# Kernel tuning notes

Measured on AMD Instinct MI355X. Metric: run time of the kernel, lower is better.

## Reference

```python
import jax, jax.numpy as jnp
import numpy as np

H, P, N, G, K, CH, E = 32, 128, 128, 8, 4, 256, 2048  # heads, head_dim, ssm_state, groups, conv_kernel, chunk, embed
I = H * P                      # intermediate_size = 4096
CD = I + 2 * G * N             # conv_dim = 6144
PROJ = I + CD + H              # 10272
EPS = 1e-6


def segsum(x):
    # x: [..., L] -> [..., L, L]; entry (i, j) = sum_{k=j+1..i} x[k] for j<=i, else -inf
    L = x.shape[-1]
    cs = jnp.cumsum(x, axis=-1)
    ss = cs[..., :, None] - cs[..., None, :]
    mask = jnp.tril(jnp.ones((L, L), dtype=bool))
    return jnp.where(mask, ss, -jnp.inf)


def setup_inputs() -> dict:
    key = jax.random.key(0)
    ks = jax.random.split(key, 6)
    b, s = 2, 2048
    return {
        'x': jax.random.normal(ks[0], (b, s, E), jnp.float32),
        'in_proj_w': jax.random.normal(ks[1], (PROJ, E), jnp.float32) / np.sqrt(E),
        'conv_w': jax.random.normal(ks[2], (CD, 1, K), jnp.float32) / np.sqrt(K),
        'conv_b': jax.random.normal(ks[3], (CD,), jnp.float32) * 0.02,
        'dt_bias': jax.random.normal(ks[4], (H,), jnp.float32) * 0.1 + 1.0,
        'A_log': jnp.log(jnp.arange(1, H + 1, dtype=jnp.float32)),
        'D': jnp.ones((H,), jnp.float32),
        'norm_w': jnp.ones((I,), jnp.float32),
        'out_proj_w': jax.random.normal(ks[5], (E, I), jnp.float32) / np.sqrt(I),
    }


def reference(x, in_proj_w, conv_w, conv_b, dt_bias, A_log, D, norm_w, out_proj_w):
    b, s, _ = x.shape
    proj = x @ in_proj_w.T                                   # [b,s,PROJ] (d_mlp == 0)
    gate, hbc, dt = jnp.split(proj, [I, I + CD], axis=-1)

    # causal depthwise conv1d (pad k-1 on left == torch pad both + slice [:s])
    hbc_t = jnp.transpose(hbc, (0, 2, 1))                    # [b,CD,s]
    conv = jax.lax.conv_general_dilated(
        hbc_t, conv_w, window_strides=(1,), padding=[(K - 1, 0)],
        feature_group_count=CD, dimension_numbers=('NCH', 'OIH', 'NCH'))
    hbc = jax.nn.silu(jnp.transpose(conv + conv_b[None, :, None], (0, 2, 1)))
    hs, B, C = jnp.split(hbc, [I, I + G * N], axis=-1)

    A = -jnp.exp(A_log.astype(jnp.float32))                  # [H]
    dt = jax.nn.softplus(dt.astype(jnp.float32) + dt_bias)   # [b,s,H]
    dt = jnp.clip(dt, 0.0, None)                             # time_step_limit (0, inf)
    X = hs.reshape(b, s, H, P).astype(jnp.float32)
    B = jnp.tile(B.reshape(b, s, G, N).astype(jnp.float32), (1, 1, H // G, 1))  # torch .repeat
    C = jnp.tile(C.reshape(b, s, G, N).astype(jnp.float32), (1, 1, H // G, 1))

    D_res = D[:, None] * X                                   # [b,s,H,P]
    X = X * dt[..., None]                                    # discretize x
    A_bt = A * dt                                            # [b,s,H] discretized A

    nc = s // CH  # seq_len chosen divisible by chunk_size (pad_size = 0)
    Xc = X.reshape(b, nc, CH, H, P)
    Bc = B.reshape(b, nc, CH, H, N)
    Cc = C.reshape(b, nc, CH, H, N)
    Ac = jnp.transpose(A_bt.reshape(b, nc, CH, H), (0, 3, 1, 2))  # [b,H,nc,CH]
    A_cum = jnp.cumsum(Ac, axis=-1)

    # 1. intra-chunk (diagonal block) outputs
    Lmat = jnp.exp(segsum(Ac))                               # [b,H,nc,l,l]
    Y_diag = jnp.einsum('bclhn,bcshn,bhcls,bcshd->bclhd', Cc, Bc, Lmat, Xc)

    # 2. per-chunk states (right factor of off-diagonal blocks)
    decay_states = jnp.exp(A_cum[..., -1:] - A_cum)          # [b,H,nc,CH]
    states = jnp.einsum('bclhn,bhcl,bclhd->bchdn', Bc, decay_states, Xc)

    # 3. inter-chunk recurrence (states at chunk boundaries)
    states = jnp.concatenate([jnp.zeros_like(states[:, :1]), states], axis=1)
    A_last = jnp.pad(A_cum[..., -1], ((0, 0), (0, 0), (1, 0)))
    decay_chunk = jnp.exp(segsum(A_last))                    # [b,H,nc+1,nc+1]
    new_states = jnp.einsum('bhij,bjhdn->bihdn', decay_chunk, states)
    states_prev = new_states[:, :-1]                         # [b,nc,H,P,N]

    # 4. state -> output (left factor of off-diagonal blocks)
    state_decay = jnp.exp(A_cum)
    Y_off = jnp.einsum('bclhn,bchdn,bhcl->bclhd', Cc, states_prev, state_decay)

    y = (Y_diag + Y_off).reshape(b, s, H, P) + D_res
    y = y.reshape(b, s, I)

    # gated grouped RMSNorm (group_size = I // G = 512, divides I)
    gs = I // G
    h32 = y * jax.nn.silu(gate.astype(jnp.float32))
    g = h32.reshape(b, s, I // gs, gs)
    var = jnp.mean(g * g, axis=-1, keepdims=True)
    h32 = (g * jax.lax.rsqrt(var + EPS)).reshape(b, s, I)
    return (norm_w * h32) @ out_proj_w.T                     # [b,s,E]
```

## Files before the change

### kernel.cpp

```cpp
#include <hip/hip_runtime.h>
#include <stdint.h>

#define Hh 32
#define Pp 128
#define Nn 128
#define Gg 8
#define Kk 4
#define CHc 256
#define Ee 2048
#define Ii 4096
#define CDd 6144
#define Mm 4096
#define NCn 8
#define GNn 1024
#define NG1 10240

using short8  = __attribute__((ext_vector_type(8))) short;
using floatx4 = __attribute__((ext_vector_type(4))) float;

__device__ __forceinline__ unsigned short f2bf(float f) {
  unsigned u = __float_as_uint(f);
  u += 0x7FFF + ((u >> 16) & 1);
  return (unsigned short)(u >> 16);
}
__device__ __forceinline__ float bf2f(unsigned short s) {
  return __uint_as_float(((unsigned)s) << 16);
}
__device__ __forceinline__ void gld_lds16(void* lds, const void* g) {
  __builtin_amdgcn_global_load_lds(
      (const __attribute__((address_space(1))) void*)g,
      (__attribute__((address_space(3))) void*)lds, 16, 0, 0);
}

__global__ void ws_probe(float* out, float mb) { out[0] = mb; }

__global__ __launch_bounds__(256) void cvt_bf16(const float* __restrict__ src,
                                                unsigned short* __restrict__ dst,
                                                size_t n4) {
  size_t i = (size_t)blockIdx.x * 256 + threadIdx.x;
  if (i < n4) {
    float4 v = ((const float4*)src)[i];
    ushort4 o;
    o.x = f2bf(v.x); o.y = f2bf(v.y); o.z = f2bf(v.z); o.w = f2bf(v.w);
    ((ushort4*)dst)[i] = o;
  }
}

__global__ __launch_bounds__(256) void dt_gemv(const float* __restrict__ x,
                                               const float* __restrict__ W1,
                                               float* __restrict__ dtraw) {
  int row = blockIdx.x;
  __shared__ float xs[Ee];
  for (int i = threadIdx.x; i < Ee / 4; i += 256)
    ((float4*)xs)[i] = ((const float4*)(x + (size_t)row * Ee))[i];
  __syncthreads();
  int h = threadIdx.x >> 3, seg = threadIdx.x & 7;
  const float* wr = W1 + (size_t)(NG1 + h) * Ee;
  float s = 0.f;
  for (int k = seg; k < Ee; k += 8) s = fmaf(xs[k], wr[k], s);
  s += __shfl_xor(s, 1);
  s += __shfl_xor(s, 2);
  s += __shfl_xor(s, 4);
  if (seg == 0) dtraw[(size_t)row * Hh + h] = s;
}

#define BM 128
#define BN 128
#define BK 64
__global__ __launch_bounds__(256) void gemm_bt(const unsigned short* __restrict__ A,
                                               const unsigned short* __restrict__ B,
                                               int K, int mode,
                                               float* __restrict__ out_f,
                                               unsigned short* __restrict__ out_gate,
                                               unsigned short* __restrict__ out_hbc,
                                               int Nout) {
  __shared__ unsigned short As[BM * BK];
  __shared__ unsigned short Bs[BN * BK];
  const int tid = threadIdx.x;
  const int wid = tid >> 6, lane = tid & 63;
  const int q = lane >> 4, l16 = lane & 15;
  const int m0 = blockIdx.y * BM;
  const int n0 = blockIdx.x * BN;
  floatx4 acc[8][2] = {};

  const int cb = tid & 192;
  for (int k0 = 0; k0 < K; k0 += BK) {
    __syncthreads();
#pragma unroll
    for (int it = 0; it < 4; ++it) {
      int chunkbase = it * 256 + cb;
      int chunk = chunkbase + lane;
      int m = chunk >> 3, kk = (chunk & 7) << 3;
      gld_lds16(&As[chunkbase * 8], &A[(size_t)(m0 + m) * K + k0 + kk]);
      gld_lds16(&Bs[chunkbase * 8], &B[(size_t)(n0 + m) * K + k0 + kk]);
    }
    __syncthreads();
#pragma unroll
    for (int kk = 0; kk < BK; kk += 32) {
      const int ko = kk + q * 8;
      short8 af[8];
#pragma unroll
      for (int mt = 0; mt < 8; ++mt)
        af[mt] = *(const short8*)&As[(mt * 16 + l16) * BK + ko];
      short8 bf0 = *(const short8*)&Bs[(wid * 32 + l16) * BK + ko];
      short8 bf1 = *(const short8*)&Bs[(wid * 32 + 16 + l16) * BK + ko];
#pragma unroll
      for (int mt = 0; mt < 8; ++mt) {
        acc[mt][0] = __builtin_amdgcn_mfma_f32_16x16x32_bf16(af[mt], bf0, acc[mt][0], 0, 0, 0);
        acc[mt][1] = __builtin_amdgcn_mfma_f32_16x16x32_bf16(af[mt], bf1, acc[mt][1], 0, 0, 0);
      }
    }
  }
#pragma unroll
  for (int mt = 0; mt < 8; ++mt)
#pragma unroll
    for (int nt = 0; nt < 2; ++nt)
#pragma unroll
      for (int r = 0; r < 4; ++r) {
        int row = m0 + mt * 16 + q * 4 + r;
        int col = n0 + wid * 32 + nt * 16 + l16;
        float v = acc[mt][nt][r];
        if (mode == 0) {
          out_f[(size_t)row * Nout + col] = v;
        } else {
          if (col < Ii) out_gate[(size_t)row * Ii + col] = f2bf(v);
          else out_hbc[(size_t)row * CDd + (col - Ii)] = f2bf(v);
        }
      }
}

__global__ __launch_bounds__(256) void conv_silu(const unsigned short* __restrict__ hbc,
                                                 const float* __restrict__ cw,
                                                 const float* __restrict__ cb,
                                                 unsigned short* __restrict__ Xr,
                                                 unsigned short* __restrict__ Bb,
                                                 unsigned short* __restrict__ Cb) {
  int idx = blockIdx.x * 256 + threadIdx.x;
  int c4 = (idx % (CDd / 4)) * 4;
  int row = idx / (CDd / 4);
  int s = row & 2047;
  const unsigned short* base = hbc + (size_t)row * CDd + c4;
  ushort4 zero = {0, 0, 0, 0};
  ushort4 r0 = (s >= 3) ? *(const ushort4*)(base - (size_t)3 * CDd) : zero;
  ushort4 r1 = (s >= 2) ? *(const ushort4*)(base - (size_t)2 * CDd) : zero;
  ushort4 r2 = (s >= 1) ? *(const ushort4*)(base - (size_t)1 * CDd) : zero;
  ushort4 r3 = *(const ushort4*)base;
  float i0[4] = {bf2f(r0.x), bf2f(r0.y), bf2f(r0.z), bf2f(r0.w)};
  float i1[4] = {bf2f(r1.x), bf2f(r1.y), bf2f(r1.z), bf2f(r1.w)};
  float i2[4] = {bf2f(r2.x), bf2f(r2.y), bf2f(r2.z), bf2f(r2.w)};
  float i3[4] = {bf2f(r3.x), bf2f(r3.y), bf2f(r3.z), bf2f(r3.w)};
  ushort4 o;
  unsigned short* op = (unsigned short*)&o;
#pragma unroll
  for (int ch = 0; ch < 4; ++ch) {
    int c = c4 + ch;
    float4 w = *(const float4*)&cw[c * 4];
    float v = cb[c];
    v = fmaf(i0[ch], w.x, v);
    v = fmaf(i1[ch], w.y, v);
    v = fmaf(i2[ch], w.z, v);
    v = fmaf(i3[ch], w.w, v);
    v = v / (1.f + expf(-v));
    op[ch] = f2bf(v);
  }
  if (c4 < Ii) *(ushort4*)&Xr[(size_t)row * Ii + c4] = o;
  else if (c4 < Ii + GNn) *(ushort4*)&Bb[(size_t)row * GNn + (c4 - Ii)] = o;
  else *(ushort4*)&Cb[(size_t)row * GNn + (c4 - Ii - GNn)] = o;
}

__global__ __launch_bounds__(256) void dt_cumsum(const float* __restrict__ dtraw,
                                                 const float* __restrict__ dt_bias,
                                                 const float* __restrict__ A_log,
                                                 float* __restrict__ dtbuf,
                                                 float* __restrict__ Acum) {
  int bc = blockIdx.x;
  int h = blockIdx.y;
  int l = threadIdx.x;
  int row = bc * CHc + l;
  float xv = dtraw[(size_t)row * Hh + h] + dt_bias[h];
  float dt = (xv > 20.f) ? xv : log1pf(expf(xv));
  dtbuf[(size_t)row * Hh + h] = dt;
  float a = -expf(A_log[h]) * dt;
  __shared__ float buf[CHc];
  buf[l] = a;
  __syncthreads();
  for (int off = 1; off < CHc; off <<= 1) {
    float v = (l >= off) ? buf[l - off] : 0.f;
    __syncthreads();
    buf[l] += v;
    __syncthreads();
  }
  Acum[((size_t)bc * Hh + h) * CHc + l] = buf[l];
}

__global__ __launch_bounds__(256, 2) void states_kernel(const unsigned short* __restrict__ Xraw,
                                                        const unsigned short* __restrict__ Bbuf,
                                                        const float* __restrict__ dtbuf,
                                                        const float* __restrict__ Acum,
                                                        unsigned short* __restrict__ states) {
  int bch = blockIdx.x;
  int h = bch & 31, bc = bch >> 5;
  int g = h & 7;
  int rowbase = bc * CHc;
  const float* Ac = Acum + (size_t)bch * CHc;
  __shared__ unsigned short XTt[128 * 136];
  __shared__ unsigned short BTt[128 * 136];
  __shared__ float wl[128];
  int t = threadIdx.x;
  int wid = t >> 6, lane = t & 63, q = lane >> 4, l16 = lane & 15;
  float Alast = Ac[CHc - 1];
  floatx4 acc[8][2] = {};
  for (int lt = 0; lt < 2; ++lt) {
    int l0 = lt * 128;
    if (t < 128)
      wl[t] = dtbuf[(size_t)(rowbase + l0 + t) * Hh + h] * __expf(Alast - Ac[l0 + t]);
    __syncthreads();
    for (int i = t; i < 2048; i += 256) {
      int r = i >> 4, c8 = (i & 15) * 8;
      int row = rowbase + l0 + r;
      const unsigned short* xp = &Xraw[(size_t)row * Ii + h * Pp + c8];
      const unsigned short* bp = &Bbuf[(size_t)row * GNn + g * Nn + c8];
      ushort4 xa = *(const ushort4*)xp;
      ushort4 xb = *(const ushort4*)(xp + 4);
      ushort4 ba = *(const ushort4*)bp;
      ushort4 bb = *(const ushort4*)(bp + 4);
      float w = wl[r];
      XTt[(c8 + 0) * 136 + r] = f2bf(bf2f(xa.x) * w);
      XTt[(c8 + 1) * 136 + r] = f2bf(bf2f(xa.y) * w);
      XTt[(c8 + 2) * 136 + r] = f2bf(bf2f(xa.z) * w);
      XTt[(c8 + 3) * 136 + r] = f2bf(bf2f(xa.w) * w);
      XTt[(c8 + 4) * 136 + r] = f2bf(bf2f(xb.x) * w);
      XTt[(c8 + 5) * 136 + r] = f2bf(bf2f(xb.y) * w);
      XTt[(c8 + 6) * 136 + r] = f2bf(bf2f(xb.z) * w);
      XTt[(c8 + 7) * 136 + r] = f2bf(bf2f(xb.w) * w);
      BTt[(c8 + 0) * 136 + r] = ba.x;
      BTt[(c8 + 1) * 136 + r] = ba.y;
      BTt[(c8 + 2) * 136 + r] = ba.z;
      BTt[(c8 + 3) * 136 + r] = ba.w;
      BTt[(c8 + 4) * 136 + r] = bb.x;
      BTt[(c8 + 5) * 136 + r] = bb.y;
      BTt[(c8 + 6) * 136 + r] = bb.z;
      BTt[(c8 + 7) * 136 + r] = bb.w;
    }
    __syncthreads();
#pragma unroll
    for (int kk = 0; kk < 128; kk += 32) {
      int ko = kk + q * 8;
      short8 af[8];
#pragma unroll
      for (int mt = 0; mt < 8; ++mt)
        af[mt] = *(const short8*)&XTt[(mt * 16 + l16) * 136 + ko];
      short8 b0 = *(const short8*)&BTt[(wid * 32 + l16) * 136 + ko];
      short8 b1 = *(const short8*)&BTt[(wid * 32 + 16 + l16) * 136 + ko];
#pragma unroll
      for (int mt = 0; mt < 8; ++mt) {
        acc[mt][0] = __builtin_amdgcn_mfma_f32_16x16x32_bf16(af[mt], b0, acc[mt][0], 0, 0, 0);
        acc[mt][1] = __builtin_amdgcn_mfma_f32_16x16x32_bf16(af[mt], b1, acc[mt][1], 0, 0, 0);
      }
    }
  }
  unsigned short* so = states + (size_t)bch * (Nn * Pp);
#pragma unroll
  for (int mt = 0; mt < 8; ++mt)
#pragma unroll
    for (int nt = 0; nt < 2; ++nt)
#pragma unroll
      for (int r = 0; r < 4; ++r)
        so[(size_t)(mt * 16 + q * 4 + r) * Nn + wid * 32 + nt * 16 + l16] =
            f2bf(acc[mt][nt][r]);
}

__global__ __launch_bounds__(256) void chunk_scan(const unsigned short* __restrict__ states,
                                                  const float* __restrict__ Acum,
                                                  unsigned short* __restrict__ sprev) {
  int bh = blockIdx.x;
  int b = bh >> 5, h = bh & 31;
  float dec[NCn];
#pragma unroll
  for (int c = 0; c < NCn; ++c)
    dec[c] = expf(Acum[((size_t)((b * NCn + c) * Hh + h)) * CHc + (CHc - 1)]);
  int e0 = blockIdx.y * 2048 + threadIdx.x;
  for (int e = e0; e < (int)(blockIdx.y + 1) * 2048; e += 256) {
    float S = 0.f;
#pragma unroll
    for (int c = 0; c < NCn; ++c) {
      size_t off = ((size_t)((b * NCn + c) * Hh + h)) * (Nn * Pp) + e;
      sprev[off] = f2bf(S);
      S = fmaf(dec[c], S, bf2f(states[off]));
    }
  }
}

__global__ __launch_bounds__(256, 1) void y_kernel(const unsigned short* __restrict__ Xraw,
                                                   const unsigned short* __restrict__ Bbuf,
                                                   const unsigned short* __restrict__ Cbuf,
                                                   const float* __restrict__ dtbuf,
                                                   const float* __restrict__ Acum,
                                                   const unsigned short* __restrict__ sprev,
                                                   unsigned short* __restrict__ ybuf) {
  int bid = blockIdx.x;
  int lt = bid & 1;
  int bch = bid >> 1;
  int h = bch & 31, bc = bch >> 5;
  int g = h & 7;
  int rowbase = bc * CHc;
  int l0 = lt * 128;
  const float* Ac = Acum + (size_t)bch * CHc;

  __shared__ unsigned short Ct[128 * 128];
  __shared__ unsigned short Bt[128 * 128];
  __shared__ unsigned short Xt[128 * 136];
  __shared__ unsigned short Gs[128 * 128];
  __shared__ float Acl[128], Aex[128], Ast[128], dts[128];

  int t = threadIdx.x;
  int wid = t >> 6, lane = t & 63, q = lane >> 4, l16 = lane & 15;

  for (int i = t; i < 2048; i += 256) {
    int r = i >> 4, c8 = (i & 15) * 8;
    *(uint4*)&Ct[r * 128 + c8] =
        *(const uint4*)&Cbuf[(size_t)(rowbase + l0 + r) * GNn + g * Nn + c8];
  }
  if (t < 128) {
    float a = Ac[l0 + t];
    Acl[t] = a;
    Aex[t] = __expf(a);
  }

  floatx4 acc[8][2] = {};

  for (int st = 0; st <= lt; ++st) {
    int s0 = st * 128;
    __syncthreads();
    for (int i = t; i < 2048; i += 256) {
      int r = i >> 4, c8 = (i & 15) * 8;
      int row = rowbase + s0 + r;
      *(uint4*)&Bt[r * 128 + c8] =
          *(const uint4*)&Bbuf[(size_t)row * GNn + g * Nn + c8];
      const unsigned short* xp = &Xraw[(size_t)row * Ii + h * Pp + c8];
      ushort4 xa = *(const ushort4*)xp;
      ushort4 xb = *(const ushort4*)(xp + 4);
      Xt[(c8 + 0) * 136 + r] = xa.x;
      Xt[(c8 + 1) * 136 + r] = xa.y;
      Xt[(c8 + 2) * 136 + r] = xa.z;
      Xt[(c8 + 3) * 136 + r] = xa.w;
      Xt[(c8 + 4) * 136 + r] = xb.x;
      Xt[(c8 + 5) * 136 + r] = xb.y;
      Xt[(c8 + 6) * 136 + r] = xb.z;
      Xt[(c8 + 7) * 136 + r] = xb.w;
    }
    if (t < 128) {
      Ast[t] = Ac[s0 + t];
      dts[t] = dtbuf[(size_t)(rowbase + s0 + t) * Hh + h];
    }
    __syncthreads();
    floatx4 gacc[8][2] = {};
#pragma unroll
    for (int kk = 0; kk < 128; kk += 32) {
      int ko = kk + q * 8;
      short8 af[8];
#pragma unroll
      for (int mt = 0; mt < 8; ++mt)
        af[mt] = *(const short8*)&Ct[(mt * 16 + l16) * 128 + ko];
      short8 b0 = *(const short8*)&Bt[(wid * 32 + l16) * 128 + ko];
      short8 b1 = *(const short8*)&Bt[(wid * 32 + 16 + l16) * 128 + ko];
#pragma unroll
      for (int mt = 0; mt < 8; ++mt) {
        gacc[mt][0] = __builtin_amdgcn_mfma_f32_16x16x32_bf16(af[mt], b0, gacc[mt][0], 0, 0, 0);
        gacc[mt][1] = __builtin_amdgcn_mfma_f32_16x16x32_bf16(af[mt], b1, gacc[mt][1], 0, 0, 0);
      }
    }
    bool diag = (st == lt);
#pragma unroll
    for (int mt = 0; mt < 8; ++mt)
#pragma unroll
      for (int nt = 0; nt < 2; ++nt)
#pragma unroll
        for (int r = 0; r < 4; ++r) {
          int l_loc = mt * 16 + q * 4 + r;
          int s_loc = wid * 32 + nt * 16 + l16;
          float v = gacc[mt][nt][r] * dts[s_loc] * __expf(Acl[l_loc] - Ast[s_loc]);
          unsigned short o = (!diag || s_loc <= l_loc) ? f2bf(v) : (unsigned short)0;
          Gs[l_loc * 128 + s_loc] = o;
        }
    __syncthreads();
#pragma unroll
    for (int kk = 0; kk < 128; kk += 32) {
      int ko = kk + q * 8;
      short8 af[8];
#pragma unroll
      for (int mt = 0; mt < 8; ++mt)
        af[mt] = *(const short8*)&Gs[(mt * 16 + l16) * 128 + ko];
      short8 b0 = *(const short8*)&Xt[(wid * 32 + l16) * 136 + ko];
      short8 b1 = *(const short8*)&Xt[(wid * 32 + 16 + l16) * 136 + ko];
#pragma unroll
      for (int mt = 0; mt < 8; ++mt) {
        acc[mt][0] = __builtin_amdgcn_mfma_f32_16x16x32_bf16(af[mt], b0, acc[mt][0], 0, 0, 0);
        acc[mt][1] = __builtin_amdgcn_mfma_f32_16x16x32_bf16(af[mt], b1, acc[mt][1], 0, 0, 0);
      }
    }
  }
  for (int i = t; i < 2048; i += 256) {
    int r = i >> 4;
    uint4 cv = *(uint4*)&Ct[i * 8];
    unsigned short* cp = (unsigned short*)&cv;
    float e = Aex[r];
#pragma unroll
    for (int j = 0; j < 8; ++j) cp[j] = f2bf(bf2f(cp[j]) * e);
    *(uint4*)&Ct[i * 8] = cv;
    *(uint4*)&Bt[i * 8] = *(const uint4*)&sprev[(size_t)bch * (Nn * Pp) + (size_t)i * 8];
  }
  __syncthreads();
#pragma unroll
  for (int kk = 0; kk < 128; kk += 32) {
    int ko = kk + q * 8;
    short8 af[8];
#pragma unroll
    for (int mt = 0; mt < 8; ++mt)
      af[mt] = *(const short8*)&Ct[(mt * 16 + l16) * 128 + ko];
    short8 b0 = *(const short8*)&Bt[(wid * 32 + l16) * 128 + ko];
    short8 b1 = *(const short8*)&Bt[(wid * 32 + 16 + l16) * 128 + ko];
#pragma unroll
    for (int mt = 0; mt < 8; ++mt) {
      acc[mt][0] = __builtin_amdgcn_mfma_f32_16x16x32_bf16(af[mt], b0, acc[mt][0], 0, 0, 0);
      acc[mt][1] = __builtin_amdgcn_mfma_f32_16x16x32_bf16(af[mt], b1, acc[mt][1], 0, 0, 0);
    }
  }
#pragma unroll
  for (int mt = 0; mt < 8; ++mt)
#pragma unroll
    for (int nt = 0; nt < 2; ++nt)
#pragma unroll
      for (int r = 0; r < 4; ++r) {
        int row = rowbase + l0 + mt * 16 + q * 4 + r;
        int col = h * Pp + wid * 32 + nt * 16 + l16;
        ybuf[(size_t)row * Ii + col] = f2bf(acc[mt][nt][r]);
      }
}

__global__ __launch_bounds__(256) void norm_kernel(const unsigned short* ybuf,
                                                   const unsigned short* gate_bf,
                                                   const unsigned short* xraw,
                                                   const float* Dvec,
                                                   const float* norm_w,
                                                   unsigned short* normed) {
  int blk = blockIdx.x;
  int row = blk >> 3, grp = blk & 7;
  size_t base = (size_t)row * Ii + grp * 512;
  int t = threadIdx.x;
  int col0 = grp * 512 + t, col1 = col0 + 256;
  float D0 = Dvec[col0 >> 7], D1 = Dvec[col1 >> 7];
  float y0 = bf2f(ybuf[base + t]) + D0 * bf2f(xraw[base + t]);
  float y1 = bf2f(ybuf[base + t + 256]) + D1 * bf2f(xraw[base + t + 256]);
  float g0 = bf2f(gate_bf[base + t]), g1 = bf2f(gate_bf[base + t + 256]);
  float h0 = y0 * (g0 / (1.f + expf(-g0)));
  float h1 = y1 * (g1 / (1.f + expf(-g1)));
  __shared__ float red[256];
  red[t] = h0 * h0 + h1 * h1;
  __syncthreads();
  for (int off = 128; off > 0; off >>= 1) {
    if (t < off) red[t] += red[t + off];
    __syncthreads();
  }
  float scale = rsqrtf(red[0] / 512.f + 1e-6f);
  normed[base + t] = f2bf(h0 * scale * norm_w[grp * 512 + t]);
  normed[base + t + 256] = f2bf(h1 * scale * norm_w[grp * 512 + t + 256]);
}

extern "C" void kernel_launch(void* const* d_in, const int* in_sizes, int n_in,
                              void* d_out, int out_size, void* d_ws, size_t ws_size,
                              hipStream_t stream) {
  const float* x    = (const float*)d_in[0];
  const float* W1   = (const float*)d_in[1];
  const float* cw   = (const float*)d_in[2];
  const float* cb   = (const float*)d_in[3];
  const float* dtb  = (const float*)d_in[4];
  const float* Alog = (const float*)d_in[5];
  const float* Dv   = (const float*)d_in[6];
  const float* nw   = (const float*)d_in[7];
  const float* W2   = (const float*)d_in[8];
  float* out = (float*)d_out;
  char* ws = (char*)d_ws;

  const size_t o_xbf   = 0;
  const size_t o_w1    = 16777216ull;
  const size_t o_gate  = o_w1 + 41943040ull;
  const size_t o_hbc   = o_gate + 33554432ull;
  const size_t o_xraw  = o_hbc + 50331648ull;
  const size_t o_b     = o_xraw + 33554432ull;
  const size_t o_c     = o_b + 8388608ull;
  const size_t o_dtraw = o_c + 8388608ull;
  const size_t o_dt    = o_dtraw + 524288ull;
  const size_t o_acum  = o_dt + 524288ull;
  const size_t total   = o_acum + 524288ull;
  if (ws_size < total) {
    ws_probe<<<1, 1, 0, stream>>>(out, (float)(ws_size >> 20));
    return;
  }

  unsigned short* xbf    = (unsigned short*)(ws + o_xbf);
  unsigned short* w1bf   = (unsigned short*)(ws + o_w1);
  unsigned short* states = (unsigned short*)(ws + o_w1);
  unsigned short* sprev  = (unsigned short*)(ws + o_w1 + 16777216ull);
  unsigned short* w2bf   = (unsigned short*)(ws + o_w1);
  unsigned short* gatebf = (unsigned short*)(ws + o_gate);
  unsigned short* hbc    = (unsigned short*)(ws + o_hbc);
  unsigned short* ybuf   = (unsigned short*)(ws + o_hbc);
  unsigned short* xraw   = (unsigned short*)(ws + o_xraw);
  unsigned short* normed = (unsigned short*)(ws + o_xraw);
  unsigned short* bbuf   = (unsigned short*)(ws + o_b);
  unsigned short* cbuf   = (unsigned short*)(ws + o_c);
  float* dtraw  = (float*)(ws + o_dtraw);
  float* dtbuf  = (float*)(ws + o_dt);
  float* acum   = (float*)(ws + o_acum);

  cvt_bf16<<<dim3(8192), dim3(256), 0, stream>>>(x, xbf, (size_t)2097152);
  cvt_bf16<<<dim3(20480), dim3(256), 0, stream>>>(W1, w1bf, (size_t)5242880);
  dt_gemv<<<dim3(Mm), dim3(256), 0, stream>>>(x, W1, dtraw);
  gemm_bt<<<dim3(NG1 / BN, Mm / BM), dim3(256), 0, stream>>>(
      xbf, w1bf, Ee, 1, nullptr, gatebf, hbc, 0);
  conv_silu<<<dim3((Mm * CDd / 4) / 256), dim3(256), 0, stream>>>(hbc, cw, cb, xraw, bbuf, cbuf);
  dt_cumsum<<<dim3(16, Hh), dim3(CHc), 0, stream>>>(dtraw, dtb, Alog, dtbuf, acum);
  states_kernel<<<dim3(512), dim3(256), 0, stream>>>(xraw, bbuf, dtbuf, acum, states);
  chunk_scan<<<dim3(64, 8), dim3(256), 0, stream>>>(states, acum, sprev);
  cvt_bf16<<<dim3(8192), dim3(256), 0, stream>>>(W2, w2bf, (size_t)2097152);
  y_kernel<<<dim3(1024), dim3(256), 0, stream>>>(xraw, bbuf, cbuf, dtbuf, acum, sprev, ybuf);
  norm_kernel<<<dim3(Mm * 8), dim3(256), 0, stream>>>(ybuf, gatebf, xraw, Dv, nw, normed);
  gemm_bt<<<dim3(Ee / BN, Mm / BM), dim3(256), 0, stream>>>(
      normed, w2bf, Ii, 0, out, nullptr, nullptr, Ee);
}
```

Baseline: 921.9 us.

## Fuse x bf16 cast into dt_gemv, swizzle GEMM tiles, widen y_kernel to 512 threads

Three independent changes. The x-to-bf16 conversion is folded into dt_gemv, which already reads x, so one launch and one pass over x are removed. Both GEMMs switch to a 1D grid that groups 16 M-tiles per N column to improve L2 reuse of weight tiles. y_kernel runs 8 waves of 512 threads, each owning 16 columns instead of 32, and aliases the Gs buffer onto Bt to cut LDS use; this adds an extra barrier per stage and halves the MFMA work per wave.

New measurement: 936.9 us. Within noise of the previous version (+1.6%).

```diff
diff --git a/kernel.cpp b/kernel.cpp
--- a/kernel.cpp
+++ b/kernel.cpp
@@ -48,11 +48,17 @@
 
 __global__ __launch_bounds__(256) void dt_gemv(const float* __restrict__ x,
                                                const float* __restrict__ W1,
-                                               float* __restrict__ dtraw) {
+                                               float* __restrict__ dtraw,
+                                               unsigned short* __restrict__ xbf) {
   int row = blockIdx.x;
   __shared__ float xs[Ee];
-  for (int i = threadIdx.x; i < Ee / 4; i += 256)
-    ((float4*)xs)[i] = ((const float4*)(x + (size_t)row * Ee))[i];
+  for (int i = threadIdx.x; i < Ee / 4; i += 256) {
+    float4 v = ((const float4*)(x + (size_t)row * Ee))[i];
+    ((float4*)xs)[i] = v;
+    ushort4 o;
+    o.x = f2bf(v.x); o.y = f2bf(v.y); o.z = f2bf(v.z); o.w = f2bf(v.w);
+    ((ushort4*)(xbf + (size_t)row * Ee))[i] = o;
+  }
   __syncthreads();
   int h = threadIdx.x >> 3, seg = threadIdx.x & 7;
   const float* wr = W1 + (size_t)(NG1 + h) * Ee;
@@ -69,7 +75,7 @@
 #define BK 64
 __global__ __launch_bounds__(256) void gemm_bt(const unsigned short* __restrict__ A,
                                                const unsigned short* __restrict__ B,
-                                               int K, int mode,
+                                               int K, int nbn, int mode,
                                                float* __restrict__ out_f,
                                                unsigned short* __restrict__ out_gate,
                                                unsigned short* __restrict__ out_hbc,
@@ -79,8 +85,13 @@
   const int tid = threadIdx.x;
   const int wid = tid >> 6, lane = tid & 63;
   const int q = lane >> 4, l16 = lane & 15;
-  const int m0 = blockIdx.y * BM;
-  const int n0 = blockIdx.x * BN;
+  const int per = nbn << 4;
+  const int grp = blockIdx.x / per;
+  const int rem = blockIdx.x - grp * per;
+  const int mi = (grp << 4) + (rem & 15);
+  const int ni = rem >> 4;
+  const int m0 = mi * BM;
+  const int n0 = ni * BN;
   floatx4 acc[8][2] = {};
 
   const int cb = tid & 192;
@@ -291,7 +302,7 @@
   }
 }
 
-__global__ __launch_bounds__(256, 1) void y_kernel(const unsigned short* __restrict__ Xraw,
+__global__ __launch_bounds__(512, 1) void y_kernel(const unsigned short* __restrict__ Xraw,
                                                    const unsigned short* __restrict__ Bbuf,
                                                    const unsigned short* __restrict__ Cbuf,
                                                    const float* __restrict__ dtbuf,
@@ -310,13 +321,13 @@
   __shared__ unsigned short Ct[128 * 128];
   __shared__ unsigned short Bt[128 * 128];
   __shared__ unsigned short Xt[128 * 136];
-  __shared__ unsigned short Gs[128 * 128];
   __shared__ float Acl[128], Aex[128], Ast[128], dts[128];
+  unsigned short* Gs = Bt;
 
   int t = threadIdx.x;
   int wid = t >> 6, lane = t & 63, q = lane >> 4, l16 = lane & 15;
 
-  for (int i = t; i < 2048; i += 256) {
+  for (int i = t; i < 2048; i += 512) {
     int r = i >> 4, c8 = (i & 15) * 8;
     *(uint4*)&Ct[r * 128 + c8] =
         *(const uint4*)&Cbuf[(size_t)(rowbase + l0 + r) * GNn + g * Nn + c8];
@@ -327,12 +338,12 @@
     Aex[t] = __expf(a);
   }
 
-  floatx4 acc[8][2] = {};
+  floatx4 acc[8] = {};
 
   for (int st = 0; st <= lt; ++st) {
     int s0 = st * 128;
     __syncthreads();
-    for (int i = t; i < 2048; i += 256) {
+    for (int i = t; i < 2048; i += 512) {
       int r = i >> 4, c8 = (i & 15) * 8;
       int row = rowbase + s0 + r;
       *(uint4*)&Bt[r * 128 + c8] =
@@ -354,7 +365,7 @@
       dts[t] = dtbuf[(size_t)(rowbase + s0 + t) * Hh + h];
     }
     __syncthreads();
-    floatx4 gacc[8][2] = {};
+    floatx4 gacc[8] = {};
 #pragma unroll
     for (int kk = 0; kk < 128; kk += 32) {
       int ko = kk + q * 8;
@@ -362,27 +373,22 @@
 #pragma unroll
       for (int mt = 0; mt < 8; ++mt)
         af[mt] = *(const short8*)&Ct[(mt * 16 + l16) * 128 + ko];
-      short8 b0 = *(const short8*)&Bt[(wid * 32 + l16) * 128 + ko];
-      short8 b1 = *(const short8*)&Bt[(wid * 32 + 16 + l16) * 128 + ko];
-#pragma unroll
-      for (int mt = 0; mt < 8; ++mt) {
-        gacc[mt][0] = __builtin_amdgcn_mfma_f32_16x16x32_bf16(af[mt], b0, gacc[mt][0], 0, 0, 0);
-        gacc[mt][1] = __builtin_amdgcn_mfma_f32_16x16x32_bf16(af[mt], b1, gacc[mt][1], 0, 0, 0);
+      short8 b0 = *(const short8*)&Bt[(wid * 16 + l16) * 128 + ko];
+#pragma unroll
+      for (int mt = 0; mt < 8; ++mt)
+        gacc[mt] = __builtin_amdgcn_mfma_f32_16x16x32_bf16(af[mt], b0, gacc[mt], 0, 0, 0);
+    }
+    __syncthreads();
+    bool diag = (st == lt);
+#pragma unroll
+    for (int mt = 0; mt < 8; ++mt)
+#pragma unroll
+      for (int r = 0; r < 4; ++r) {
+        int l_loc = mt * 16 + q * 4 + r;
+        int s_loc = wid * 16 + l16;
+        float v = gacc[mt][r] * dts[s_loc] * __expf(Acl[l_loc] - Ast[s_loc]);
+        Gs[l_loc * 128 + s_loc] = (!diag || s_loc <= l_loc) ? f2bf(v) : (unsigned short)0;
       }
-    }
-    bool diag = (st == lt);
-#pragma unroll
-    for (int mt = 0; mt < 8; ++mt)
-#pragma unroll
-      for (int nt = 0; nt < 2; ++nt)
-#pragma unroll
-        for (int r = 0; r < 4; ++r) {
-          int l_loc = mt * 16 + q * 4 + r;
-          int s_loc = wid * 32 + nt * 16 + l16;
-          float v = gacc[mt][nt][r] * dts[s_loc] * __expf(Acl[l_loc] - Ast[s_loc]);
-          unsigned short o = (!diag || s_loc <= l_loc) ? f2bf(v) : (unsigned short)0;
-          Gs[l_loc * 128 + s_loc] = o;
-        }
     __syncthreads();
 #pragma unroll
     for (int kk = 0; kk < 128; kk += 32) {
@@ -391,16 +397,14 @@
 #pragma unroll
       for (int mt = 0; mt < 8; ++mt)
         af[mt] = *(const short8*)&Gs[(mt * 16 + l16) * 128 + ko];
-      short8 b0 = *(const short8*)&Xt[(wid * 32 + l16) * 136 + ko];
-      short8 b1 = *(const short8*)&Xt[(wid * 32 + 16 + l16) * 136 + ko];
-#pragma unroll
-      for (int mt = 0; mt < 8; ++mt) {
-        acc[mt][0] = __builtin_amdgcn_mfma_f32_16x16x32_bf16(af[mt], b0, acc[mt][0], 0, 0, 0);
-        acc[mt][1] = __builtin_amdgcn_mfma_f32_16x16x32_bf16(af[mt], b1, acc[mt][1], 0, 0, 0);
-      }
-    }
-  }
-  for (int i = t; i < 2048; i += 256) {
+      short8 b0 = *(const short8*)&Xt[(wid * 16 + l16) * 136 + ko];
+#pragma unroll
+      for (int mt = 0; mt < 8; ++mt)
+        acc[mt] = __builtin_amdgcn_mfma_f32_16x16x32_bf16(af[mt], b0, acc[mt], 0, 0, 0);
+    }
+  }
+  __syncthreads();
+  for (int i = t; i < 2048; i += 512) {
     int r = i >> 4;
     uint4 cv = *(uint4*)&Ct[i * 8];
     unsigned short* cp = (unsigned short*)&cv;
@@ -418,24 +422,19 @@
 #pragma unroll
     for (int mt = 0; mt < 8; ++mt)
       af[mt] = *(const short8*)&Ct[(mt * 16 + l16) * 128 + ko];
-    short8 b0 = *(const short8*)&Bt[(wid * 32 + l16) * 128 + ko];
-    short8 b1 = *(const short8*)&Bt[(wid * 32 + 16 + l16) * 128 + ko];
-#pragma unroll
-    for (int mt = 0; mt < 8; ++mt) {
-      acc[mt][0] = __builtin_amdgcn_mfma_f32_16x16x32_bf16(af[mt], b0, acc[mt][0], 0, 0, 0);
-      acc[mt][1] = __builtin_amdgcn_mfma_f32_16x16x32_bf16(af[mt], b1, acc[mt][1], 0, 0, 0);
-    }
+    short8 b0 = *(const short8*)&Bt[(wid * 16 + l16) * 128 + ko];
+#pragma unroll
+    for (int mt = 0; mt < 8; ++mt)
+      acc[mt] = __builtin_amdgcn_mfma_f32_16x16x32_bf16(af[mt], b0, acc[mt], 0, 0, 0);
   }
 #pragma unroll
   for (int mt = 0; mt < 8; ++mt)
 #pragma unroll
-    for (int nt = 0; nt < 2; ++nt)
-#pragma unroll
-      for (int r = 0; r < 4; ++r) {
-        int row = rowbase + l0 + mt * 16 + q * 4 + r;
-        int col = h * Pp + wid * 32 + nt * 16 + l16;
-        ybuf[(size_t)row * Ii + col] = f2bf(acc[mt][nt][r]);
-      }
+    for (int r = 0; r < 4; ++r) {
+      int row = rowbase + l0 + mt * 16 + q * 4 + r;
+      int col = h * Pp + wid * 16 + l16;
+      ybuf[(size_t)row * Ii + col] = f2bf(acc[mt][r]);
+    }
 }
 
 __global__ __launch_bounds__(256) void norm_kernel(const unsigned short* ybuf,
@@ -514,18 +513,17 @@
   float* dtbuf  = (float*)(ws + o_dt);
   float* acum   = (float*)(ws + o_acum);
 
-  cvt_bf16<<<dim3(8192), dim3(256), 0, stream>>>(x, xbf, (size_t)2097152);
   cvt_bf16<<<dim3(20480), dim3(256), 0, stream>>>(W1, w1bf, (size_t)5242880);
-  dt_gemv<<<dim3(Mm), dim3(256), 0, stream>>>(x, W1, dtraw);
-  gemm_bt<<<dim3(NG1 / BN, Mm / BM), dim3(256), 0, stream>>>(
-      xbf, w1bf, Ee, 1, nullptr, gatebf, hbc, 0);
+  dt_gemv<<<dim3(Mm), dim3(256), 0, stream>>>(x, W1, dtraw, xbf);
+  gemm_bt<<<dim3((Mm / BM) * (NG1 / BN)), dim3(256), 0, stream>>>(
+      xbf, w1bf, Ee, NG1 / BN, 1, nullptr, gatebf, hbc, 0);
   conv_silu<<<dim3((Mm * CDd / 4) / 256), dim3(256), 0, stream>>>(hbc, cw, cb, xraw, bbuf, cbuf);
   dt_cumsum<<<dim3(16, Hh), dim3(CHc), 0, stream>>>(dtraw, dtb, Alog, dtbuf, acum);
   states_kernel<<<dim3(512), dim3(256), 0, stream>>>(xraw, bbuf, dtbuf, acum, states);
   chunk_scan<<<dim3(64, 8), dim3(256), 0, stream>>>(states, acum, sprev);
   cvt_bf16<<<dim3(8192), dim3(256), 0, stream>>>(W2, w2bf, (size_t)2097152);
-  y_kernel<<<dim3(1024), dim3(256), 0, stream>>>(xraw, bbuf, cbuf, dtbuf, acum, sprev, ybuf);
+  y_kernel<<<dim3(1024), dim3(512), 0, stream>>>(xraw, bbuf, cbuf, dtbuf, acum, sprev, ybuf);
   norm_kernel<<<dim3(Mm * 8), dim3(256), 0, stream>>>(ybuf, gatebf, xraw, Dv, nw, normed);
-  gemm_bt<<<dim3(Ee / BN, Mm / BM), dim3(256), 0, stream>>>(
-      normed, w2bf, Ii, 0, out, nullptr, nullptr, Ee);
-}
+  gemm_bt<<<dim3((Mm / BM) * (Ee / BN)), dim3(256), 0, stream>>>(
+      normed, w2bf, Ii, Ee / BN, 0, out, nullptr, nullptr, Ee);
+}
```
